# Performance work log

Hardware: AMD Instinct MI355X
Metric: run time of the kernel (lower is better)

The kernel has to match this reference:

```python
import jax, jax.numpy as jnp
import numpy as np

LRELU_SLOPE = 0.1  # correlate_operator uses F.leaky_relu_(corr, 0.1)


def _conv2d(x, w, b):
    # x: [B,Ci,H,W], w: [Co,Ci,kh,kw], stride 1, padding SAME (=padding=1 for 3x3)
    y = jax.lax.conv_general_dilated(x, w, (1, 1), 'SAME',
                                     dimension_numbers=('NCHW', 'OIHW', 'NCHW'))
    return y + b[None, :, None, None]


def correlate(x1, x2):
    # spatial_correlation_sample(x1, x2, kernel_size=3, patch_size=1, stride=1,
    # padding=1): with patch_size=1 the only displacement is (0,0), so the cost
    # volume is a 3x3 window sum of the per-pixel channel dot product.
    # Then divided by C and leaky_relu(0.1) as in correlate_operator.
    prod = jnp.sum(x1 * x2, axis=1, keepdims=True)  # [B,1,H,W]
    box = jnp.ones((1, 1, 3, 3), prod.dtype)
    corr = jax.lax.conv_general_dilated(prod, box, (1, 1), 'SAME',
                                        dimension_numbers=('NCHW', 'OIHW', 'NCHW'))
    corr = corr / x1.shape[1]
    return jnp.where(corr > 0, corr, LRELU_SLOPE * corr)


def deform_conv2d(x, offset, w):
    # mmcv DeformConv2d: kernel 3x3, stride 1, pad 1, dilation 1, deform_groups=1,
    # bias=False. offset: [B, 2*kh*kw, H, W], per kernel tap k: (dy_k, dx_k).
    B, Cin, H, W = x.shape
    O, _, kh, kw = w.shape
    K = kh * kw
    off = offset.reshape(B, K, 2, H, W)
    dy, dx = off[:, :, 0], off[:, :, 1]  # [B,K,H,W]
    ky, kx = jnp.meshgrid(jnp.arange(kh), jnp.arange(kw), indexing='ij')
    # sampling position: p + p_k + offset_k (pad=1 cancels the kernel-center shift)
    y = jnp.arange(H, dtype=x.dtype)[None, None, :, None] \
        + (ky.reshape(-1) - kh // 2).astype(x.dtype)[None, :, None, None] + dy
    xx = jnp.arange(W, dtype=x.dtype)[None, None, None, :] \
        + (kx.reshape(-1) - kw // 2).astype(x.dtype)[None, :, None, None] + dx
    y0 = jnp.floor(y)
    x0 = jnp.floor(xx)
    wy = (y - y0)[:, None]   # [B,1,K,H,W]
    wx = (xx - x0)[:, None]
    y0i = y0.astype(jnp.int32)
    x0i = x0.astype(jnp.int32)
    xf = x.reshape(B, Cin, H * W)

    def gather(yi, xi):
        valid = (yi >= 0) & (yi < H) & (xi >= 0) & (xi < W)  # zero padding outside
        idx = jnp.clip(yi, 0, H - 1) * W + jnp.clip(xi, 0, W - 1)
        v = jnp.take_along_axis(xf, idx.reshape(B, 1, K * H * W), axis=2)
        return v.reshape(B, Cin, K, H, W) * valid.astype(x.dtype)[:, None]

    v00 = gather(y0i, x0i)
    v01 = gather(y0i, x0i + 1)
    v10 = gather(y0i + 1, x0i)
    v11 = gather(y0i + 1, x0i + 1)
    samp = (v00 * (1 - wy) * (1 - wx) + v01 * (1 - wy) * wx
            + v10 * wy * (1 - wx) + v11 * wy * wx)  # [B,Cin,K,H,W]
    return jnp.einsum('bckhw,ock->bohw', samp, w.reshape(O, Cin, K))


def setup_inputs() -> dict:
    key = jax.random.key(0)
    ks = jax.random.split(key, 10)
    B, C, H, W = 4, 256, 64, 64
    s = 0.02
    return {
        'x_ref': jax.random.normal(ks[0], (B, C, H, W), jnp.float32),
        'x_next': jax.random.normal(ks[1], (B, C, H, W), jnp.float32),
        'w1': jax.random.normal(ks[2], (256, 1, 3, 3), jnp.float32) * s,
        'b1': jax.random.normal(ks[3], (256,), jnp.float32) * s,
        'w2': jax.random.normal(ks[4], (256, 256, 3, 3), jnp.float32) * s,
        'b2': jax.random.normal(ks[5], (256,), jnp.float32) * s,
        'w3': jax.random.normal(ks[6], (18, 256, 3, 3), jnp.float32) * s,
        'b3': jax.random.normal(ks[7], (18,), jnp.float32) * s,
        'w_dcn': jax.random.normal(ks[8], (256, 256, 3, 3), jnp.float32) * s,
        'idx': 4,
    }


def reference(x_ref, x_next, w1, b1, w2, b2, w3, b3, w_dcn, idx):
    # idx=4 -> corr_patch_size=1 (consistent with conv1 in_channels)
    corr = correlate(x_next, x_ref)                      # [B,1,H,W]
    h = jax.nn.relu(_conv2d(corr, w1, b1))               # [B,256,H,W]
    h = jax.nn.relu(_conv2d(h, w2, b2))                  # [B,256,H,W]
    offset = jax.nn.relu(_conv2d(h, w3, b3))             # [B,18,H,W]
    x_ref_cal = jax.nn.relu(deform_conv2d(x_ref, offset, w_dcn))
    return 0.5 * (x_next + x_ref_cal)
```

## Files before the change

### kernel.cpp

```cpp
#include <hip/hip_runtime.h>

typedef __attribute__((ext_vector_type(8))) short short8v;
typedef __attribute__((ext_vector_type(4))) float f32x4;
typedef __attribute__((ext_vector_type(2))) float f32x2;
typedef __attribute__((ext_vector_type(4))) unsigned int u32x4;

constexpr int Bsz = 4;
constexpr int Hh = 64, Wwd = 64;
constexpr int HWp = Hh * Wwd;
constexpr int NPIX = Bsz * HWp;
constexpr int HH = 66;
constexpr int HPIX = HH * HH;
constexpr int Kdim = 2304;
constexpr int NSTEP = 36;

constexpr size_t B_H1H  = 0;
constexpr size_t HALO_BYTES = (size_t)Bsz * HPIX * 256 * 2;
constexpr size_t B_H2H  = B_H1H + HALO_BYTES;
constexpr size_t B_XTH  = B_H2H + HALO_BYTES;
constexpr size_t B_PROD = B_XTH + HALO_BYTES;
constexpr size_t B_OFFP = B_PROD + (size_t)NPIX * 4;
constexpr size_t B_WB2  = B_OFFP + (size_t)NPIX * 32 * 4;
constexpr size_t B_WBD  = B_WB2 + (size_t)256 * Kdim * 2;
constexpr size_t B_WB3  = B_WBD + (size_t)256 * Kdim * 2;

static __device__ __forceinline__ unsigned short f2bf(float f) {
    unsigned u = __builtin_bit_cast(unsigned, f);
    u += 0x7FFFu + ((u >> 16) & 1u);
    return (unsigned short)(u >> 16);
}
static __device__ __forceinline__ unsigned cvt_pk_bf16(float lo, float hi) {
    unsigned r;
    asm("v_cvt_pk_bf16_f32 %0, %1, %2" : "=v"(r) : "v"(lo), "v"(hi));
    return r;
}
static __device__ __forceinline__ f32x2 pk_mul(f32x2 a, f32x2 b) {
    f32x2 d;
    asm("v_pk_mul_f32 %0, %1, %2" : "=v"(d) : "v"(a), "v"(b));
    return d;
}
static __device__ __forceinline__ f32x2 pk_fma(f32x2 a, f32x2 b, f32x2 c) {
    f32x2 d;
    asm("v_pk_fma_f32 %0, %1, %2, %3" : "=v"(d) : "v"(a), "v"(b), "v"(c));
    return d;
}
static __device__ __forceinline__ f32x2 unpack2(unsigned u) {
    f32x2 v;
    v.x = __builtin_bit_cast(float, u << 16);
    v.y = __builtin_bit_cast(float, u & 0xFFFF0000u);
    return v;
}
static __device__ __forceinline__ void gload_lds16(const void* g, void* l) {
    __builtin_amdgcn_global_load_lds((const __attribute__((address_space(1))) unsigned int*)g,
                                     (__attribute__((address_space(3))) unsigned int*)l, 16, 0, 0);
}
static __device__ __forceinline__ int swz(int u) {
    return (((u & 7) ^ ((u >> 3) & 7)) << 3);
}

__global__ void k_zero_ring(unsigned short* h1h, unsigned short* h2h, unsigned short* xth,
                            float* prod) {
    int blk = blockIdx.x;
    if (blk >= 3120) {
        unsigned* p = (unsigned*)prod + (size_t)(blk - 3120) * 128 + threadIdx.x;
        *p = 0;
        return;
    }
    int img = blk / 260;
    int rp = blk - img * 260;
    int buf = img >> 2, b = img & 3;
    int y, x;
    if (rp < 66) { y = 0; x = rp; }
    else if (rp < 132) { y = 65; x = rp - 66; }
    else { int s2 = rp - 132; y = 1 + (s2 >> 1); x = (s2 & 1) * 65; }
    unsigned short* base = (buf == 0) ? h1h : (buf == 1) ? h2h : xth;
    unsigned* p = (unsigned*)(base + ((size_t)b * HPIX + y * HH + x) * 256);
    p[threadIdx.x] = 0;
}

__global__ void k_prodx(const float* __restrict__ xr, const float* __restrict__ xn,
                        unsigned short* __restrict__ xth, float* __restrict__ prod) {
    __shared__ float t[32][33];
    __shared__ float red[8][33];
    int b = blockIdx.z;
    int c0 = blockIdx.y * 32;
    int y = blockIdx.x >> 1, x0 = (blockIdx.x & 1) * 32;
    int tx = threadIdx.x, ty = threadIdx.y;
    float part = 0.f;
#pragma unroll
    for (int i = 0; i < 32; i += 8) {
        size_t idx = ((size_t)b * 256 + c0 + ty + i) * HWp + y * Wwd + x0 + tx;
        float vr = xr[idx];
        float vn = xn[idx];
        t[ty + i][tx] = vr;
        part = fmaf(vr, vn, part);
    }
    red[ty][tx] = part;
    __syncthreads();
#pragma unroll
    for (int i = 0; i < 32; i += 8)
        xth[((size_t)b * HPIX + (y + 1) * HH + (x0 + ty + i + 1)) * 256 + c0 + tx] =
            f2bf(t[tx][ty + i]);
    if (ty == 0) {
        float s = red[0][tx] + red[1][tx] + red[2][tx] + red[3][tx] +
                  red[4][tx] + red[5][tx] + red[6][tx] + red[7][tx];
        atomicAdd(&prod[b * HWp + y * Wwd + x0 + tx], s);
    }
}

__global__ __launch_bounds__(256) void k_conv1c(const float* __restrict__ prod,
                                                const float* __restrict__ w1,
                                                const float* __restrict__ b1,
                                                unsigned short* __restrict__ h1h) {
    __shared__ float pp[5][36];
    __shared__ float pt[3][34];
    int px0 = blockIdx.x * 32;
    int b = px0 >> 12, y = (px0 & 4095) >> 6, x0 = px0 & 63;
    int tid = threadIdx.x;
    if (tid < 180) {
        int i = tid / 36, j = tid - i * 36;
        int yy = y - 2 + i, xx = x0 - 2 + j;
        float v = 0.f;
        if (yy >= 0 && yy < Hh && xx >= 0 && xx < Wwd) v = prod[b * HWp + yy * Wwd + xx];
        pp[i][j] = v;
    }
    __syncthreads();
    if (tid < 102) {
        int i = tid / 34, j = tid - i * 34;
        int yy = y - 1 + i, xx = x0 - 1 + j;
        float v = 0.f;
        if (yy >= 0 && yy < Hh && xx >= 0 && xx < Wwd) {
            float s = pp[i][j]     + pp[i][j + 1]     + pp[i][j + 2] +
                      pp[i + 1][j] + pp[i + 1][j + 1] + pp[i + 1][j + 2] +
                      pp[i + 2][j] + pp[i + 2][j + 1] + pp[i + 2][j + 2];
            s *= (1.0f / 256.0f);
            v = (s > 0.f) ? s : 0.1f * s;
        }
        pt[i][j] = v;
    }
    float wl[9];
#pragma unroll
    for (int k = 0; k < 9; ++k) wl[k] = w1[tid * 9 + k];
    float bias = b1[tid];
    __syncthreads();
    for (int p = 0; p < 32; ++p) {
        float acc = bias;
#pragma unroll
        for (int ky = 0; ky < 3; ++ky)
#pragma unroll
            for (int kx = 0; kx < 3; ++kx) acc = fmaf(pt[ky][p + kx], wl[ky * 3 + kx], acc);
        acc = fmaxf(acc, 0.f);
        h1h[((size_t)b * HPIX + (y + 1) * HH + (x0 + p + 1)) * 256 + tid] = f2bf(acc);
    }
}

__global__ void k_packall(const float* __restrict__ w2, const float* __restrict__ wd,
                          const float* __restrict__ w3,
                          unsigned short* __restrict__ wb2f, unsigned short* __restrict__ wbdf,
                          unsigned short* __restrict__ wb3) {
    int blk = blockIdx.x;
    if (blk < 4608) {
        const float* w = (blk < 2304) ? w2 : wd;
        unsigned short* out = (blk < 2304) ? wb2f : wbdf;
        int i = (blk % 2304) * 256 + threadIdx.x;
        int e = i & 7;
        int lane = (i >> 3) & 63;
        int mi = (i >> 9) & 1;
        int kf = (i >> 10) & 1;
        int rest = i >> 11;
        int s = rest % 36;
        int wv = rest / 36;
        int o = wv * 32 + mi * 16 + (lane & 15);
        int kk = s * 64 + (kf * 4 + (lane >> 4)) * 8 + e;
        int c = kk & 255, tap = kk >> 8;
        out[i] = f2bf(w[((size_t)o * 256 + c) * 9 + tap]);
    } else {
        int i = (blk - 4608) * 256 + threadIdx.x;
        int o = i / Kdim;
        int r = i - o * Kdim;
        int k = r >> 8, c = r & 255;
        float v = (o < 18) ? w3[((size_t)o * 256 + c) * 9 + k] : 0.f;
        wb3[i] = f2bf(v);
    }
}

__global__ __launch_bounds__(256) void k_conv2g(const unsigned short* __restrict__ h1h,
                                                const unsigned short* __restrict__ wbf,
                                                const float* __restrict__ bias,
                                                unsigned short* __restrict__ h2h) {
    __shared__ short S_s[2][64 * 64];
    const int tid = threadIdx.x;
    const int bid = blockIdx.x;
    const int lin = (bid & 7) * 64 + (bid >> 3);
    const int px0 = (lin >> 1) * 64;
    const int oblk = lin & 1;
    const int b = px0 >> 12;
    const unsigned short* hb = h1h + (size_t)b * HPIX * 256;
    const int pxl = tid >> 2;
    const int px = px0 + pxl;
    const int y = (px & 4095) >> 6, x = px & 63;
    const int u0 = (tid & 3) * 2;
    const int lane = tid & 63, wv = tid >> 6;
    const int ot = oblk * 4 + wv;
    const unsigned short* wfb = wbf + (size_t)ot * NSTEP * 2048 + lane * 8;
    const unsigned short* abase0 = hb + (size_t)((y + 1) * HH + (x + 1)) * 256 + u0 * 8;

    f32x4 acc[4][2] = {};
    u32x4 wA[4], wB[4], aA0, aA1, aB0, aB1;
    float bia[2];
#pragma unroll
    for (int oi = 0; oi < 2; ++oi) bia[oi] = bias[ot * 32 + oi * 16 + (lane & 15)];

    const int wr0 = pxl * 64 + ((u0 ^ (pxl & 7)) << 3);
    const int wr1 = pxl * 64 + (((u0 + 1) ^ (pxl & 7)) << 3);

    auto WLOAD = [&](int s, u32x4 (&wreg)[4]) {
#pragma unroll
        for (int f = 0; f < 4; ++f)
            wreg[f] = *(const u32x4*)(wfb + ((size_t)s * 4 + f) * 512);
    };
    auto ALOAD = [&](int s, u32x4& a0, u32x4& a1) {
        int tap = s >> 2, chunk = s & 3;
        int aoff = ((tap / 3 - 1) * HH + (tap % 3 - 1)) * 256 + chunk * 64;
        a0 = *(const u32x4*)(abase0 + aoff);
        a1 = *(const u32x4*)(abase0 + aoff + 8);
    };

    {
        u32x4 a0, a1;
        ALOAD(0, a0, a1);
        WLOAD(0, wA);
        *(u32x4*)&S_s[0][wr0] = a0;
        *(u32x4*)&S_s[0][wr1] = a1;
        ALOAD(1, aA0, aA1);
        asm volatile("s_waitcnt lgkmcnt(0)" ::: "memory");
    }

    auto ITER = [&](int s, u32x4 (&wcur)[4], u32x4 (&wnxt)[4],
                    u32x4& aC0, u32x4& aC1, u32x4& aN0, u32x4& aN1,
                    short* SBc, short* SBn) {
        __builtin_amdgcn_s_barrier();
        __builtin_amdgcn_sched_barrier(0);
        if (s + 1 < NSTEP) {
            *(u32x4*)&SBn[wr0] = aC0;
            *(u32x4*)&SBn[wr1] = aC1;
        }
        if (s + 2 < NSTEP) ALOAD(s + 2, aN0, aN1);
        if (s + 1 < NSTEP) WLOAD(s + 1, wnxt);
        short8v af[4][2];
#pragma unroll
        for (int pi = 0; pi < 4; ++pi) {
            int row = pi * 16 + (lane & 15);
#pragma unroll
            for (int kf = 0; kf < 2; ++kf) {
                int c8 = kf * 4 + (lane >> 4);
                af[pi][kf] = *(const short8v*)&SBc[row * 64 + ((c8 ^ (row & 7)) << 3)];
            }
        }
        __builtin_amdgcn_s_setprio(1);
#pragma unroll
        for (int kf = 0; kf < 2; ++kf)
#pragma unroll
            for (int pi = 0; pi < 4; ++pi)
#pragma unroll
                for (int oi = 0; oi < 2; ++oi)
                    acc[pi][oi] = __builtin_amdgcn_mfma_f32_16x16x32_bf16(
                        af[pi][kf], __builtin_bit_cast(short8v, wcur[kf * 2 + oi]),
                        acc[pi][oi], 0, 0, 0);
        __builtin_amdgcn_s_setprio(0);
        asm volatile("s_waitcnt lgkmcnt(0)" ::: "memory");
    };

    for (int s2 = 0; s2 < NSTEP; s2 += 2) {
        ITER(s2, wA, wB, aA0, aA1, aB0, aB1, &S_s[0][0], &S_s[1][0]);
        ITER(s2 + 1, wB, wA, aB0, aB1, aA0, aA1, &S_s[1][0], &S_s[0][0]);
    }

#pragma unroll
    for (int pi = 0; pi < 4; ++pi) {
#pragma unroll
        for (int j = 0; j < 4; ++j) {
            int p2 = px0 + pi * 16 + (lane >> 4) * 4 + j;
            int yy = (p2 & 4095) >> 6, xx = p2 & 63;
            unsigned short* dst = h2h + ((size_t)b * HPIX + (yy + 1) * HH + (xx + 1)) * 256;
#pragma unroll
            for (int oi = 0; oi < 2; ++oi) {
                int o = ot * 32 + oi * 16 + (lane & 15);
                dst[o] = f2bf(fmaxf(acc[pi][oi][j] + bia[oi], 0.f));
            }
        }
    }
}

__global__ __launch_bounds__(256) void k_conv3g(const unsigned short* __restrict__ h2h,
                                                const unsigned short* __restrict__ wb,
                                                const float* __restrict__ bias,
                                                float* __restrict__ offp) {
    __shared__ short A_s[2][64 * 64];
    __shared__ short B_s[2][32 * 64];
    const int tid = threadIdx.x;
    const int px0 = blockIdx.x * 64;
    const int b = px0 >> 12;
    const unsigned short* hb = h2h + (size_t)b * HPIX * 256;

    const unsigned short* abase[2];
#pragma unroll
    for (int i = 0; i < 2; ++i) {
        int u = i * 256 + tid;
        int pxl = u >> 3;
        int pxg = px0 + pxl;
        int y = (pxg & 4095) >> 6, x = pxg & 63;
        abase[i] = hb + (size_t)((y + 1) * HH + (x + 1)) * 256 + swz(u);
    }
    const unsigned short* bbase = wb + (size_t)(tid >> 3) * Kdim + swz(tid);

    const int lane = tid & 63, wv = tid >> 6;
    f32x4 acc[2] = {};

    auto STAGE = [&](int s, int buf) {
        int tap = s >> 2, chunk = s & 3;
        int delta = ((tap / 3 - 1) * HH + (tap % 3 - 1)) * 256 + chunk * 64;
        short* Ab = &A_s[buf][0];
#pragma unroll
        for (int i = 0; i < 2; ++i) gload_lds16(abase[i] + delta, Ab + (i * 256 + tid) * 8);
        gload_lds16(bbase + s * 64, &B_s[buf][tid * 8]);
    };

    STAGE(0, 0);
    __syncthreads();
    for (int s = 0; s < NSTEP; ++s) {
        int cur = s & 1;
        if (s + 1 < NSTEP) STAGE(s + 1, cur ^ 1);
        const short* Ab = &A_s[cur][0];
        const short* Bb = &B_s[cur][0];
        short8v af[2], bf[2][2];
#pragma unroll
        for (int kf = 0; kf < 2; ++kf) {
            int row = wv * 16 + (lane & 15);
            int c8 = kf * 4 + (lane >> 4);
            af[kf] = *(const short8v*)&Ab[row * 64 + ((c8 ^ (row & 7)) << 3)];
        }
#pragma unroll
        for (int ni = 0; ni < 2; ++ni) {
            int row = ni * 16 + (lane & 15);
#pragma unroll
            for (int kf = 0; kf < 2; ++kf) {
                int c8 = kf * 4 + (lane >> 4);
                bf[ni][kf] = *(const short8v*)&Bb[row * 64 + ((c8 ^ (row & 7)) << 3)];
            }
        }
#pragma unroll
        for (int kf = 0; kf < 2; ++kf)
#pragma unroll
            for (int ni = 0; ni < 2; ++ni)
                acc[ni] = __builtin_amdgcn_mfma_f32_16x16x32_bf16(af[kf], bf[ni][kf], acc[ni], 0, 0, 0);
        __syncthreads();
    }
#pragma unroll
    for (int j = 0; j < 4; ++j) {
        int px = px0 + wv * 16 + (lane >> 4) * 4 + j;
#pragma unroll
        for (int ni = 0; ni < 2; ++ni) {
            int o = ni * 16 + (lane & 15);
            float bv = (o < 18) ? bias[o] : 0.f;
            offp[(size_t)px * 32 + o] = fmaxf(acc[ni][j] + bv, 0.f);
        }
    }
}

__global__ __launch_bounds__(512) void k_dcng(const unsigned short* __restrict__ xth,
                                              const float* __restrict__ offp,
                                              const unsigned short* __restrict__ wbf,
                                              const float* __restrict__ xn,
                                              float* __restrict__ out) {
    __shared__ short S_s[4][64 * 64];
    const int tid = threadIdx.x;
    const int bid = blockIdx.x;
    const int px0 = ((bid & 7) * 32 + (bid >> 3)) * 64;
    const int b = px0 >> 12;
    const unsigned short* xb = xth + (size_t)b * HPIX * 256;
    const int pxl = tid >> 3;
    const int px = px0 + pxl;
    const int y = (px & 4095) >> 6, x = px & 63;
    const int u0 = tid & 7;
    const int lane = tid & 63, wv = tid >> 6;
    const unsigned short* wfb = wbf + (size_t)wv * NSTEP * 2048 + lane * 8;
    const float2* offv = (const float2*)offp;

    f32x4 acc[2][4] = {};
    u32x4 wA[2][4], wB[2][4];
    u32x4 g[2][4];
    const int wr0 = pxl * 64 + ((u0 ^ (pxl & 7)) << 3);

    const unsigned short* pcorner[4];
    f32x2 wpair[4];
    float2 offn;

    auto SETUP = [&](int tap, float dyo, float dxo) {
        int ky = tap / 3 - 1, kx = tap % 3 - 1;
        float ypos = (float)(y + ky) + dyo;
        float xpos = (float)(x + kx) + dxo;
        float y0f = floorf(ypos), x0f = floorf(xpos);
        float wy = ypos - y0f, wx = xpos - x0f;
        int y0 = (int)y0f, x0 = (int)x0f;
        bool y0v = (y0 >= 0) && (y0 < Hh), y1v = (y0 + 1 >= 0) && (y0 + 1 < Hh);
        bool x0v = (x0 >= 0) && (x0 < Wwd), x1v = (x0 + 1 >= 0) && (x0 + 1 < Wwd);
        int hy0 = min(max(y0, -1), 64) + 1, hy1 = min(max(y0 + 1, -1), 64) + 1;
        int hx0 = min(max(x0, -1), 64) + 1, hx1 = min(max(x0 + 1, -1), 64) + 1;
        float w0 = (1.f - wy) * (1.f - wx) * (float)(y0v && x0v);
        float w1 = (1.f - wy) * wx * (float)(y0v && x1v);
        float w2 = wy * (1.f - wx) * (float)(y1v && x0v);
        float w3 = wy * wx * (float)(y1v && x1v);
        wpair[0] = (f32x2){w0, w0};
        wpair[1] = (f32x2){w1, w1};
        wpair[2] = (f32x2){w2, w2};
        wpair[3] = (f32x2){w3, w3};
        pcorner[0] = xb + (size_t)((hy0 * HH + hx0) * 256) + u0 * 8;
        pcorner[1] = xb + (size_t)((hy0 * HH + hx1) * 256) + u0 * 8;
        pcorner[2] = xb + (size_t)((hy1 * HH + hx0) * 256) + u0 * 8;
        pcorner[3] = xb + (size_t)((hy1 * HH + hx1) * 256) + u0 * 8;
    };
    auto WLOAD = [&](int s, u32x4 (&wreg)[4]) {
#pragma unroll
        for (int f = 0; f < 4; ++f)
            wreg[f] = *(const u32x4*)(wfb + ((size_t)s * 4 + f) * 512);
    };
    auto GISSUE = [&](int s, u32x4 (&gr)[4]) {
        const int nco = (s & 3) * 64;
#pragma unroll
        for (int c = 0; c < 4; ++c) gr[c] = *(const u32x4*)(pcorner[c] + nco);
    };
    auto COMBINE_WRITE = [&](u32x4 (&gr)[4], short* SBn) {
        u32x4 res;
#pragma unroll
        for (int qd = 0; qd < 4; ++qd) {
            f32x2 a = pk_mul(unpack2(gr[0][qd]), wpair[0]);
            a = pk_fma(unpack2(gr[1][qd]), wpair[1], a);
            a = pk_fma(unpack2(gr[2][qd]), wpair[2], a);
            a = pk_fma(unpack2(gr[3][qd]), wpair[3], a);
            res[qd] = cvt_pk_bf16(a.x, a.y);
        }
        *(u32x4*)&SBn[wr0] = res;
    };

    {
        float2 o0 = offv[(size_t)px * 16];
        SETUP(0, o0.x, o0.y);
        u32x4 g0[4], g1[4];
        GISSUE(0, g0);
        GISSUE(1, g1);
        WLOAD(0, wA[0]);
        WLOAD(1, wA[1]);
        COMBINE_WRITE(g0, &S_s[0][0]);
        COMBINE_WRITE(g1, &S_s[1][0]);
        GISSUE(2, g[0]);
        GISSUE(3, g[1]);
        offn = offv[(size_t)px * 16 + 1];
        asm volatile("s_waitcnt lgkmcnt(0)" ::: "memory");
    }

    auto ITER2 = [&](int s, u32x4 (&wcur)[2][4], u32x4 (&wnxt)[2][4], short* SBc, short* SBn) {
        __builtin_amdgcn_s_barrier();
        __builtin_amdgcn_sched_barrier(0);
        if (s + 2 < NSTEP) {
            COMBINE_WRITE(g[0], SBn);
            COMBINE_WRITE(g[1], SBn + 64 * 64);
        }
        if ((s & 3) == 0 && s + 4 < NSTEP)
            SETUP((s + 4) >> 2, offn.x, offn.y);
        if ((s & 3) == 2 && ((s + 8) >> 2) < 9)
            offn = offv[(size_t)px * 16 + ((s + 8) >> 2)];
        if (s + 4 < NSTEP) {
            GISSUE(s + 4, g[0]);
            GISSUE(s + 5, g[1]);
        }
        if (s + 2 < NSTEP) {
            WLOAD(s + 2, wnxt[0]);
            WLOAD(s + 3, wnxt[1]);
        }
#pragma unroll
        for (int half = 0; half < 2; ++half) {
            const short* SB = SBc + half * 64 * 64;
            short8v sf[4][2];
#pragma unroll
            for (int ni = 0; ni < 4; ++ni) {
                int row = ni * 16 + (lane & 15);
#pragma unroll
                for (int kf = 0; kf < 2; ++kf) {
                    int c8 = kf * 4 + (lane >> 4);
                    sf[ni][kf] = *(const short8v*)&SB[row * 64 + ((c8 ^ (row & 7)) << 3)];
                }
            }
            __builtin_amdgcn_s_setprio(1);
#pragma unroll
            for (int kf = 0; kf < 2; ++kf)
#pragma unroll
                for (int mi = 0; mi < 2; ++mi)
#pragma unroll
                    for (int ni = 0; ni < 4; ++ni)
                        acc[mi][ni] = __builtin_amdgcn_mfma_f32_16x16x32_bf16(
                            __builtin_bit_cast(short8v, wcur[half][kf * 2 + mi]), sf[ni][kf],
                            acc[mi][ni], 0, 0, 0);
            __builtin_amdgcn_s_setprio(0);
        }
        asm volatile("s_waitcnt lgkmcnt(0)" ::: "memory");
    };

    for (int s4 = 0; s4 < NSTEP; s4 += 4) {
        ITER2(s4, wA, wB, &S_s[0][0], &S_s[2][0]);
        ITER2(s4 + 2, wB, wA, &S_s[2][0], &S_s[0][0]);
    }

#pragma unroll
    for (int mi = 0; mi < 2; ++mi) {
        int o = wv * 32 + mi * 16 + (lane >> 4) * 4;
#pragma unroll
        for (int j = 0; j < 4; ++j) {
            size_t rowbase = ((size_t)b * 256 + o + j) * HWp;
#pragma unroll
            for (int ni = 0; ni < 4; ++ni) {
                int p2 = (px0 + ni * 16 + (lane & 15)) & 4095;
                size_t idx = rowbase + p2;
                out[idx] = 0.5f * (xn[idx] + fmaxf(acc[mi][ni][j], 0.f));
            }
        }
    }
}

extern "C" void kernel_launch(void* const* d_in, const int* in_sizes, int n_in,
                              void* d_out, int out_size, void* d_ws, size_t ws_size,
                              hipStream_t stream) {
    const float* x_ref  = (const float*)d_in[0];
    const float* x_next = (const float*)d_in[1];
    const float* w1 = (const float*)d_in[2];
    const float* b1 = (const float*)d_in[3];
    const float* w2 = (const float*)d_in[4];
    const float* b2 = (const float*)d_in[5];
    const float* w3 = (const float*)d_in[6];
    const float* b3 = (const float*)d_in[7];
    const float* wd = (const float*)d_in[8];
    float* out = (float*)d_out;
    char* ws = (char*)d_ws;

    unsigned short* h1h = (unsigned short*)(ws + B_H1H);
    unsigned short* h2h = (unsigned short*)(ws + B_H2H);
    unsigned short* xth = (unsigned short*)(ws + B_XTH);
    float* prod = (float*)(ws + B_PROD);
    float* offp = (float*)(ws + B_OFFP);
    unsigned short* wb2f = (unsigned short*)(ws + B_WB2);
    unsigned short* wbdf = (unsigned short*)(ws + B_WBD);
    unsigned short* wb3  = (unsigned short*)(ws + B_WB3);

    k_zero_ring<<<3120 + 128, 128, 0, stream>>>(h1h, h2h, xth, prod);
    k_prodx<<<dim3(128, 8, Bsz), dim3(32, 8), 0, stream>>>(x_ref, x_next, xth, prod);
    k_packall<<<4896, 256, 0, stream>>>(w2, wd, w3, wb2f, wbdf, wb3);
    k_conv1c<<<NPIX / 32, 256, 0, stream>>>(prod, w1, b1, h1h);
    k_conv2g<<<512, 256, 0, stream>>>(h1h, wb2f, b2, h2h);
    k_conv3g<<<256, 256, 0, stream>>>(h2h, wb3, b3, offp);
    k_dcng<<<256, 512, 0, stream>>>(xth, offp, wbdf, x_next, out);
}
```

Before: 108.9 us.

## Process two K-steps per barrier in conv2 GEMM with deeper LDS buffering

The conv2 implicit-GEMM main loop now handles two K-steps per iteration, staging two 64x64 A tiles per LDS buffer (LDS doubled to four slots) and holding weights for two steps in registers. This halves the number of block barriers and waitcnt drains, and issues more global loads per sync to hide latency. The cost is higher register pressure (twice the weight and A prefetch registers) and twice the LDS, which can lower occupancy. The edit to the conv3 kernel only reads B_s directly instead of through an alias pointer.

Result: no change. 107.5 us (-1.3%).

```diff
diff --git a/kernel.cpp b/kernel.cpp
--- a/kernel.cpp
+++ b/kernel.cpp
@@ -188,7 +188,7 @@
                                                 const unsigned short* __restrict__ wbf,
                                                 const float* __restrict__ bias,
                                                 unsigned short* __restrict__ h2h) {
-    __shared__ short S_s[2][64 * 64];
+    __shared__ short S_s[4][64 * 64];
     const int tid = threadIdx.x;
     const int bid = blockIdx.x;
     const int lin = (bid & 7) * 64 + (bid >> 3);
@@ -206,7 +206,8 @@
     const unsigned short* abase0 = hb + (size_t)((y + 1) * HH + (x + 1)) * 256 + u0 * 8;
 
     f32x4 acc[4][2] = {};
-    u32x4 wA[4], wB[4], aA0, aA1, aB0, aB1;
+    u32x4 wA[2][4], wB[2][4];
+    u32x4 aP[4], aQ[4];
     float bia[2];
 #pragma unroll
     for (int oi = 0; oi < 2; ++oi) bia[oi] = bias[ot * 32 + oi * 16 + (lane & 15)];
@@ -227,53 +228,69 @@
     };
 
     {
-        u32x4 a0, a1;
+        u32x4 a0, a1, a2, a3;
         ALOAD(0, a0, a1);
-        WLOAD(0, wA);
+        ALOAD(1, a2, a3);
+        WLOAD(0, wA[0]);
+        WLOAD(1, wA[1]);
         *(u32x4*)&S_s[0][wr0] = a0;
         *(u32x4*)&S_s[0][wr1] = a1;
-        ALOAD(1, aA0, aA1);
+        *(u32x4*)&S_s[1][wr0] = a2;
+        *(u32x4*)&S_s[1][wr1] = a3;
+        ALOAD(2, aP[0], aP[1]);
+        ALOAD(3, aP[2], aP[3]);
         asm volatile("s_waitcnt lgkmcnt(0)" ::: "memory");
     }
 
-    auto ITER = [&](int s, u32x4 (&wcur)[4], u32x4 (&wnxt)[4],
-                    u32x4& aC0, u32x4& aC1, u32x4& aN0, u32x4& aN1,
-                    short* SBc, short* SBn) {
+    auto ITER2 = [&](int s, u32x4 (&wcur)[2][4], u32x4 (&wnxt)[2][4],
+                     u32x4 (&aC)[4], u32x4 (&aN)[4], short* SBc, short* SBn) {
         __builtin_amdgcn_s_barrier();
         __builtin_amdgcn_sched_barrier(0);
-        if (s + 1 < NSTEP) {
-            *(u32x4*)&SBn[wr0] = aC0;
-            *(u32x4*)&SBn[wr1] = aC1;
-        }
-        if (s + 2 < NSTEP) ALOAD(s + 2, aN0, aN1);
-        if (s + 1 < NSTEP) WLOAD(s + 1, wnxt);
-        short8v af[4][2];
-#pragma unroll
-        for (int pi = 0; pi < 4; ++pi) {
-            int row = pi * 16 + (lane & 15);
-#pragma unroll
-            for (int kf = 0; kf < 2; ++kf) {
-                int c8 = kf * 4 + (lane >> 4);
-                af[pi][kf] = *(const short8v*)&SBc[row * 64 + ((c8 ^ (row & 7)) << 3)];
+        if (s + 2 < NSTEP) {
+            *(u32x4*)&SBn[wr0] = aC[0];
+            *(u32x4*)&SBn[wr1] = aC[1];
+            *(u32x4*)&SBn[64 * 64 + wr0] = aC[2];
+            *(u32x4*)&SBn[64 * 64 + wr1] = aC[3];
+        }
+        if (s + 4 < NSTEP) {
+            ALOAD(s + 4, aN[0], aN[1]);
+            ALOAD(s + 5, aN[2], aN[3]);
+        }
+        if (s + 2 < NSTEP) {
+            WLOAD(s + 2, wnxt[0]);
+            WLOAD(s + 3, wnxt[1]);
+        }
+#pragma unroll
+        for (int half = 0; half < 2; ++half) {
+            const short* SB = SBc + half * 64 * 64;
+            short8v af[4][2];
+#pragma unroll
+            for (int pi = 0; pi < 4; ++pi) {
+                int row = pi * 16 + (lane & 15);
+#pragma unroll
+                for (int kf = 0; kf < 2; ++kf) {
+                    int c8 = kf * 4 + (lane >> 4);
+                    af[pi][kf] = *(const short8v*)&SB[row * 64 + ((c8 ^ (row & 7)) << 3)];
+                }
             }
-        }
-        __builtin_amdgcn_s_setprio(1);
-#pragma unroll
-        for (int kf = 0; kf < 2; ++kf)
-#pragma unroll
-            for (int pi = 0; pi < 4; ++pi)
-#pragma unroll
-                for (int oi = 0; oi < 2; ++oi)
-                    acc[pi][oi] = __builtin_amdgcn_mfma_f32_16x16x32_bf16(
-                        af[pi][kf], __builtin_bit_cast(short8v, wcur[kf * 2 + oi]),
-                        acc[pi][oi], 0, 0, 0);
-        __builtin_amdgcn_s_setprio(0);
+            __builtin_amdgcn_s_setprio(1);
+#pragma unroll
+            for (int kf = 0; kf < 2; ++kf)
+#pragma unroll
+                for (int pi = 0; pi < 4; ++pi)
+#pragma unroll
+                    for (int oi = 0; oi < 2; ++oi)
+                        acc[pi][oi] = __builtin_amdgcn_mfma_f32_16x16x32_bf16(
+                            af[pi][kf], __builtin_bit_cast(short8v, wcur[half][kf * 2 + oi]),
+                            acc[pi][oi], 0, 0, 0);
+            __builtin_amdgcn_s_setprio(0);
+        }
         asm volatile("s_waitcnt lgkmcnt(0)" ::: "memory");
     };
 
-    for (int s2 = 0; s2 < NSTEP; s2 += 2) {
-        ITER(s2, wA, wB, aA0, aA1, aB0, aB1, &S_s[0][0], &S_s[1][0]);
-        ITER(s2 + 1, wB, wA, aB0, aB1, aA0, aA1, &S_s[1][0], &S_s[0][0]);
+    for (int s4 = 0; s4 < NSTEP; s4 += 4) {
+        ITER2(s4, wA, wB, aP, aQ, &S_s[0][0], &S_s[2][0]);
+        ITER2(s4 + 2, wB, wA, aQ, aP, &S_s[2][0], &S_s[0][0]);
     }
 
 #pragma unroll
@@ -346,7 +363,7 @@
 #pragma unroll
             for (int kf = 0; kf < 2; ++kf) {
                 int c8 = kf * 4 + (lane >> 4);
-                bf[ni][kf] = *(const short8v*)&Bb[row * 64 + ((c8 ^ (row & 7)) << 3)];
+                bf[ni][kf] = *(const short8v*)&B_s[cur][row * 64 + ((c8 ^ (row & 7)) << 3)];
             }
         }
 #pragma unroll
```
